# Kernel tuning notes

Measured on AMD Instinct MI355X. Metric: run time of the kernel, lower is better.

Reference implementation:

```python
import jax, jax.numpy as jnp
import numpy as np

B, E, F = 16384, 128, 6
ITEM_V, CATE_V, HIST = 91718, 11, 50
I_IDX, J_IDX = np.triu_indices(F, k=1)  # 15 field pairs, loop order (0,1),(0,2),...
EPS = 1e-5


def _xavier(key, shape):
    fan_in, fan_out = shape[0], shape[-1]
    std = (2.0 / (fan_in + fan_out)) ** 0.5
    return std * jax.random.normal(key, shape, dtype=jnp.float32)


def setup_inputs() -> dict:
    key = jax.random.key(0)
    ks = jax.random.split(key, 20)
    inp = {
        'item_id': jax.random.randint(ks[0], (B,), 0, ITEM_V),
        'item_emb_d128': jax.random.normal(ks[1], (B, 128), dtype=jnp.float32),
        'likes_level': jax.random.randint(ks[2], (B,), 0, CATE_V),
        'views_level': jax.random.randint(ks[3], (B,), 0, CATE_V),
        'item_seq': jax.random.randint(ks[4], (B, HIST), 0, ITEM_V),
        # learned parameters
        'item_emb': 0.05 * jax.random.normal(ks[5], (ITEM_V, E), dtype=jnp.float32),
        'cate_emb': 0.05 * jax.random.normal(ks[6], (CATE_V, E), dtype=jnp.float32),
        'mm_W': _xavier(ks[7], (128, E)), 'mm_b': jnp.zeros((E,), jnp.float32),
        'ln_g': jnp.ones((E,), jnp.float32), 'ln_b': jnp.zeros((E,), jnp.float32),
        'se_W1': _xavier(ks[8], (F, F // 2)), 'se_b1': jnp.zeros((F // 2,), jnp.float32),
        'se_W2': _xavier(ks[9], (F // 2, F)), 'se_b2': jnp.zeros((F,), jnp.float32),
        'bi_W': _xavier(ks[10], (E, E)),
        'mlp_W1': _xavier(ks[11], (21 * E, 512)), 'mlp_b1': jnp.zeros((512,), jnp.float32),
        'bn1_g': jnp.ones((512,), jnp.float32), 'bn1_b': jnp.zeros((512,), jnp.float32),
        'bn1_rm': jnp.zeros((512,), jnp.float32), 'bn1_rv': jnp.ones((512,), jnp.float32),
        'mlp_W2': _xavier(ks[12], (512, 256)), 'mlp_b2': jnp.zeros((256,), jnp.float32),
        'bn2_g': jnp.ones((256,), jnp.float32), 'bn2_b': jnp.zeros((256,), jnp.float32),
        'bn2_rm': jnp.zeros((256,), jnp.float32), 'bn2_rv': jnp.ones((256,), jnp.float32),
        'mlp_W3': _xavier(ks[13], (256, 1)), 'mlp_b3': jnp.zeros((1,), jnp.float32),
    }
    return inp


def _forward(item_id, item_emb_d128, likes_level, views_level, item_seq,
             item_emb, cate_emb, mm_W, mm_b, ln_g, ln_b,
             se_W1, se_b1, se_W2, se_b2, bi_W,
             mlp_W1, mlp_b1, bn1_g, bn1_b, bn1_rm, bn1_rv,
             mlp_W2, mlp_b2, bn2_g, bn2_b, bn2_rm, bn2_rv,
             mlp_W3, mlp_b3):
    b = item_id.shape[0]
    tab = item_emb.at[0].set(0.0)  # padding_idx=0
    like_feat = cate_emb[likes_level]
    view_feat = cate_emb[views_level]
    item_feat = tab[item_id]
    # mm_proj: Linear -> LayerNorm -> ReLU
    mm = item_emb_d128 @ mm_W + mm_b
    mu = mm.mean(-1, keepdims=True)
    var = jnp.var(mm, axis=-1, keepdims=True)
    mm = jax.nn.relu((mm - mu) / jnp.sqrt(var + EPS) * ln_g + ln_b)
    # masked mean pooling over history
    seq_emb = tab[item_seq]                               # (B, HIST, E)
    valid = (item_seq != 0).astype(seq_emb.dtype)
    seq_sum = (seq_emb * valid[..., None]).sum(1)
    cnt = jnp.clip(valid.sum(1, keepdims=True), 1.0)
    hist_feat = seq_sum / cnt
    user_feat = jnp.zeros((b, E), seq_emb.dtype)
    x = jnp.stack([user_feat, like_feat, view_feat, item_feat, mm, hist_feat], axis=1)  # (B,6,E)
    # SENet
    z = x.mean(-1)
    w = jax.nn.sigmoid(jax.nn.relu(z @ se_W1 + se_b1) @ se_W2 + se_b2)
    xs = x * w[:, :, None]
    # bilinear 'all'
    xw = jnp.einsum('bfe,ed->bfd', xs, bi_W)
    p = xs[:, I_IDX, :] * xw[:, J_IDX, :]                 # (B,15,E)
    c = jnp.concatenate([xs.reshape(b, -1), p.reshape(b, -1)], axis=1)  # (B, 2688)
    # MLP head (eval mode: BN uses running stats, dropout off)
    h = c @ mlp_W1 + mlp_b1
    h = jax.nn.relu((h - bn1_rm) / jnp.sqrt(bn1_rv + EPS) * bn1_g + bn1_b)
    h = h @ mlp_W2 + mlp_b2
    h = jax.nn.relu((h - bn2_rm) / jnp.sqrt(bn2_rv + EPS) * bn2_g + bn2_b)
    logits = h @ mlp_W3 + mlp_b3
    return jax.nn.sigmoid(logits)[:, 0]


def reference(item_id, item_emb_d128, likes_level, views_level, item_seq,
              item_emb, cate_emb, mm_W, mm_b, ln_g, ln_b,
              se_W1, se_b1, se_W2, se_b2, bi_W,
              mlp_W1, mlp_b1, bn1_g, bn1_b, bn1_rm, bn1_rv,
              mlp_W2, mlp_b2, bn2_g, bn2_b, bn2_rm, bn2_rv,
              mlp_W3, mlp_b3):
    return _forward(item_id, item_emb_d128, likes_level, views_level, item_seq,
                    item_emb, cate_emb, mm_W, mm_b, ln_g, ln_b,
                    se_W1, se_b1, se_W2, se_b2, bi_W,
                    mlp_W1, mlp_b1, bn1_g, bn1_b, bn1_rm, bn1_rv,
                    mlp_W2, mlp_b2, bn2_g, bn2_b, bn2_rm, bn2_rv,
                    mlp_W3, mlp_b3)
```

## Files before the change

kernel.cpp:

```cpp
#include <hip/hip_runtime.h>
#include <hip/hip_bf16.h>

typedef __hip_bfloat16 bfloat;
typedef __bf16 bf16x8 __attribute__((ext_vector_type(8)));
typedef float f32x4 __attribute__((ext_vector_type(4)));

#define B_SZ   16384
#define E_DIM  128
#define HIST_L 50


#define IPACK 0x3221110000ULL
#define JPACK 0x3323213210ULL

__device__ __forceinline__ void gl_lds16(const void* g, void* l) {
    __builtin_amdgcn_global_load_lds(
        (const __attribute__((address_space(1))) unsigned int*)g,
        (__attribute__((address_space(3))) unsigned int*)l, 16, 0, 0);
}

__device__ __forceinline__ bf16x8 mul_bf16x8(bf16x8 a, bf16x8 b) {
    union { bf16x8 v; __hip_bfloat162 h[4]; } ua, ub, ur;
    ua.v = a; ub.v = b;
    #pragma unroll
    for (int i = 0; i < 4; ++i) ur.h[i] = __hmul2(ua.h[i], ub.h[i]);
    return ur.v;
}

template<int TB>
__global__ __launch_bounds__(256) void feat_kernel(
    const int* __restrict__ item_id,
    const int* __restrict__ likes, const int* __restrict__ views,
    const int* __restrict__ seq,
    const void* __restrict__ item_tab, const float* __restrict__ cate_emb,
    const float* __restrict__ mm,
    const float* __restrict__ ln_g, const float* __restrict__ ln_b,
    const float* __restrict__ se_W1, const float* __restrict__ se_b1,
    const float* __restrict__ se_W2, const float* __restrict__ se_b2,
    bfloat* __restrict__ xs)
{
    const int tid = threadIdx.x;
    const int r   = tid >> 7;
    const int e   = tid & 127;
    const int b   = blockIdx.x * 2 + r;
    const int w   = tid >> 6;

    __shared__ float redh[2][4][128];
    __shared__ int   seq_s[2][64];
    __shared__ float lnred[4], lnred2[4];
    __shared__ float zred[5][4];
    __shared__ float wsh[2][6];
    __shared__ int   cnt_s[2];

    if (e < 64) seq_s[r][e] = (e < HIST_L) ? seq[(size_t)b * HIST_L + e] : 0;
    __syncthreads();

    const int iid = item_id[b];
    const float like_v = cate_emb[likes[b] * 128 + e];
    const float view_v = cate_emb[views[b] * 128 + e];
    float item_v;
    if (TB) {
        const bfloat* tb = (const bfloat*)item_tab;
        item_v = __bfloat162float(tb[(size_t)iid * 128 + e]);
    } else {
        const float* tf = (const float*)item_tab;
        float raw = tf[(size_t)iid * 128 + e];
        item_v = iid ? raw : 0.f;
    }
    const float acc = mm[(size_t)b * 128 + e];

    const int q   = e >> 5;
    const int l32 = e & 31;
    float4 hs = make_float4(0.f, 0.f, 0.f, 0.f);
    if (TB) {
        const ushort* tb = (const ushort*)item_tab;
        #pragma unroll
        for (int g = 0; g < 13; ++g) {
            int s = seq_s[r][g * 4 + q];
            ushort4 v = *(const ushort4*)&tb[(size_t)s * 128 + l32 * 4];
            hs.x += __bfloat162float(__ushort_as_bfloat16(v.x));
            hs.y += __bfloat162float(__ushort_as_bfloat16(v.y));
            hs.z += __bfloat162float(__ushort_as_bfloat16(v.z));
            hs.w += __bfloat162float(__ushort_as_bfloat16(v.w));
        }
    } else {
        const float* tf = (const float*)item_tab;
        #pragma unroll
        for (int g = 0; g < 13; ++g) {
            int s = seq_s[r][g * 4 + q];
            const float4 v = *(const float4*)&tf[(size_t)s * 128 + l32 * 4];
            float m = (s != 0) ? 1.f : 0.f;
            hs.x = fmaf(v.x, m, hs.x);
            hs.y = fmaf(v.y, m, hs.y);
            hs.z = fmaf(v.z, m, hs.z);
            hs.w = fmaf(v.w, m, hs.w);
        }
    }

    {
        float v = acc;
        #pragma unroll
        for (int off = 32; off > 0; off >>= 1) v += __shfl_down(v, off, 64);
        if ((tid & 63) == 0) lnred[w] = v;
    }
    __syncthreads();
    const float mu = (lnred[2 * r] + lnred[2 * r + 1]) * (1.f / 128.f);
    const float d  = acc - mu;
    {
        float v = d * d;
        #pragma unroll
        for (int off = 32; off > 0; off >>= 1) v += __shfl_down(v, off, 64);
        if ((tid & 63) == 0) lnred2[w] = v;
    }
    redh[r][q][l32 * 4 + 0] = hs.x;
    redh[r][q][l32 * 4 + 1] = hs.y;
    redh[r][q][l32 * 4 + 2] = hs.z;
    redh[r][q][l32 * 4 + 3] = hs.w;
    if ((w & 1) == 0 && e < 64) {
        bool valid = (e < HIST_L) && (seq_s[r][e] != 0);
        unsigned long long m = __ballot(valid);
        if (e == 0) cnt_s[r] = (int)__popcll(m);
    }
    __syncthreads();
    const float var = (lnred2[2 * r] + lnred2[2 * r + 1]) * (1.f / 128.f);
    float xmm = d * rsqrtf(var + 1e-5f) * ln_g[e] + ln_b[e];
    xmm = fmaxf(xmm, 0.f);

    const int cnt = cnt_s[r] > 0 ? cnt_s[r] : 1;
    const float hist_v = (redh[r][0][e] + redh[r][1][e] +
                          redh[r][2][e] + redh[r][3][e]) / (float)cnt;

    {
        float s1 = like_v, s2 = view_v, s3 = item_v, s4 = xmm, s5 = hist_v;
        #pragma unroll
        for (int off = 32; off > 0; off >>= 1) {
            s1 += __shfl_down(s1, off, 64);
            s2 += __shfl_down(s2, off, 64);
            s3 += __shfl_down(s3, off, 64);
            s4 += __shfl_down(s4, off, 64);
            s5 += __shfl_down(s5, off, 64);
        }
        if ((tid & 63) == 0) {
            zred[0][w] = s1; zred[1][w] = s2; zred[2][w] = s3;
            zred[3][w] = s4; zred[4][w] = s5;
        }
    }
    __syncthreads();

    if (e == 0) {
        float z[6];
        z[0] = 0.f;
        #pragma unroll
        for (int f = 1; f < 6; ++f)
            z[f] = (zred[f - 1][2 * r] + zred[f - 1][2 * r + 1]) * (1.f / 128.f);
        float a[3];
        #pragma unroll
        for (int j = 0; j < 3; ++j) {
            float s = se_b1[j];
            #pragma unroll
            for (int f = 0; f < 6; ++f) s += z[f] * se_W1[f * 3 + j];
            a[j] = fmaxf(s, 0.f);
        }
        #pragma unroll
        for (int f = 0; f < 6; ++f) {
            float s = se_b2[f];
            #pragma unroll
            for (int j = 0; j < 3; ++j) s += a[j] * se_W2[j * 6 + f];
            wsh[r][f] = 1.f / (1.f + expf(-s));
        }
    }
    __syncthreads();

    bfloat* xrow = xs + (size_t)b * 640;
    xrow[0 * 128 + e] = __float2bfloat16(like_v * wsh[r][1]);
    xrow[1 * 128 + e] = __float2bfloat16(view_v * wsh[r][2]);
    xrow[2 * 128 + e] = __float2bfloat16(item_v * wsh[r][3]);
    xrow[3 * 128 + e] = __float2bfloat16(xmm    * wsh[r][4]);
    xrow[4 * 128 + e] = __float2bfloat16(hist_v * wsh[r][5]);
}

__global__ __launch_bounds__(256) void transpose_f32_bf16(
    const float* __restrict__ in, bfloat* __restrict__ out, int K, int N)
{
    int idx = blockIdx.x * 256 + threadIdx.x;
    if (idx < K * N) {
        int k = idx / N, n = idx % N;
        out[(size_t)n * K + k] = __float2bfloat16(in[idx]);
    }
}

__global__ __launch_bounds__(256) void transpose_W1c(
    const float* __restrict__ W1, bfloat* __restrict__ W1t)
{
    int idx = blockIdx.x * 256 + threadIdx.x;
    if (idx < 512 * 1920) {
        int n = idx / 1920, kk = idx % 1920;
        int orig = kk + (kk < 640 ? 128 : 768);
        W1t[idx] = __float2bfloat16(W1[(size_t)orig * 512 + n]);
    }
}

__global__ __launch_bounds__(256) void cvt_f32_bf16(
    const float* __restrict__ in, bfloat* __restrict__ out, int n8)
{
    int idx = blockIdx.x * 256 + threadIdx.x;
    if (idx < n8) {
        float4 f0 = ((const float4*)in)[idx * 2];
        float4 f1 = ((const float4*)in)[idx * 2 + 1];
        union { bf16x8 v; unsigned short s[8]; } u;
        u.s[0] = __bfloat16_as_ushort(__float2bfloat16(f0.x));
        u.s[1] = __bfloat16_as_ushort(__float2bfloat16(f0.y));
        u.s[2] = __bfloat16_as_ushort(__float2bfloat16(f0.z));
        u.s[3] = __bfloat16_as_ushort(__float2bfloat16(f0.w));
        u.s[4] = __bfloat16_as_ushort(__float2bfloat16(f1.x));
        u.s[5] = __bfloat16_as_ushort(__float2bfloat16(f1.y));
        u.s[6] = __bfloat16_as_ushort(__float2bfloat16(f1.z));
        u.s[7] = __bfloat16_as_ushort(__float2bfloat16(f1.w));
        ((bf16x8*)out)[idx] = u.v;
    }
}

__global__ __launch_bounds__(256) void cvt_emb(
    const float* __restrict__ in, bfloat* __restrict__ out, int n8)
{
    int idx = blockIdx.x * 256 + threadIdx.x;
    if (idx >= n8) return;
    if (idx < 16) {
        union { bf16x8 v; unsigned short s[8]; } z;
        #pragma unroll
        for (int i = 0; i < 8; ++i) z.s[i] = 0;
        ((bf16x8*)out)[idx] = z.v;
        return;
    }
    float4 f0 = ((const float4*)in)[idx * 2];
    float4 f1 = ((const float4*)in)[idx * 2 + 1];
    union { bf16x8 v; unsigned short s[8]; } u;
    u.s[0] = __bfloat16_as_ushort(__float2bfloat16(f0.x));
    u.s[1] = __bfloat16_as_ushort(__float2bfloat16(f0.y));
    u.s[2] = __bfloat16_as_ushort(__float2bfloat16(f0.z));
    u.s[3] = __bfloat16_as_ushort(__float2bfloat16(f0.w));
    u.s[4] = __bfloat16_as_ushort(__float2bfloat16(f1.x));
    u.s[5] = __bfloat16_as_ushort(__float2bfloat16(f1.y));
    u.s[6] = __bfloat16_as_ushort(__float2bfloat16(f1.z));
    u.s[7] = __bfloat16_as_ushort(__float2bfloat16(f1.w));
    ((bf16x8*)out)[idx] = u.v;
}

__global__ __launch_bounds__(256) void pair_kernel(
    const bfloat* __restrict__ xs, const bfloat* __restrict__ xw,
    bfloat* __restrict__ P, int total)
{
    int idx = blockIdx.x * 256 + threadIdx.x;
    if (idx >= total) return;
    int b = idx / 160, c = idx % 160;
    int pp = c >> 4, q = c & 15;
    int isl = (int)((IPACK >> (4 * pp)) & 15);
    int jsl = (int)((JPACK >> (4 * pp)) & 15);
    bf16x8 a = *(const bf16x8*)&xs[(size_t)b * 640 + isl * 128 + q * 8];
    bf16x8 w = *(const bf16x8*)&xw[((size_t)b * 4 + jsl) * 128 + q * 8];
    *(bf16x8*)&P[(size_t)b * 1280 + c * 8] = mul_bf16x8(a, w);
}

__global__ __launch_bounds__(256) void bn_pre(
    const float* __restrict__ lb1, const float* __restrict__ g1,
    const float* __restrict__ bb1, const float* __restrict__ rm1,
    const float* __restrict__ rv1,
    const float* __restrict__ lb2, const float* __restrict__ g2,
    const float* __restrict__ bb2, const float* __restrict__ rm2,
    const float* __restrict__ rv2,
    const float* __restrict__ mm_b,
    float* __restrict__ S1, float* __restrict__ T1,
    float* __restrict__ S2, float* __restrict__ T2,
    float* __restrict__ Tmm)
{
    int j = blockIdx.x * 256 + threadIdx.x;
    if (j < 512) {
        float s = g1[j] * rsqrtf(rv1[j] + 1e-5f);
        S1[j] = s;
        T1[j] = (lb1[j] - rm1[j]) * s + bb1[j];
    } else if (j < 768) {
        int k = j - 512;
        float s = g2[k] * rsqrtf(rv2[k] + 1e-5f);
        S2[k] = s;
        T2[k] = (lb2[k] - rm2[k]) * s + bb2[k];
    } else if (j < 896) {
        Tmm[j - 768] = mm_b[j - 768];
    }
}

template<int MODE, int EPI, int F32OUT>
__global__ __launch_bounds__(256) void gemm_bt(
    const void* __restrict__ A, const bfloat* __restrict__ A2,
    const bfloat* __restrict__ Bt, void* __restrict__ C,
    int M, int N, int K,
    const float* __restrict__ S, const float* __restrict__ T)
{
    __shared__ __align__(16) short As[3][64 * 64];
    __shared__ __align__(16) short Bs[3][64 * 64];

    const int tid  = threadIdx.x;
    const int bm   = blockIdx.x * 64;
    const int bn   = blockIdx.y * 64;
    const int wave = tid >> 6;
    const int lane = tid & 63;
    const int wm   = (wave >> 1) * 32;
    const int wn   = (wave & 1) * 32;

    const short* Ag  = (const short*)A;
    const short* A2g = (const short*)A2;
    const short* Bg  = (const short*)Bt;

    f32x4 acc[2][2];
    #pragma unroll
    for (int i = 0; i < 2; ++i)
        #pragma unroll
        for (int j = 0; j < 2; ++j)
            acc[i][j] = (f32x4){0.f, 0.f, 0.f, 0.f};

    const int srow = tid >> 3;
    const int sck  = tid & 7;

    auto stage = [&](int buf, int kt) {
        #pragma unroll
        for (int rr = 0; rr < 2; ++rr) {
            int row = srow + rr * 32;
            int g   = sck ^ (row & 7);
            gl_lds16(&Bg[(long)(bn + row) * K + kt + g * 8],
                     &Bs[buf][row * 64 + sck * 8]);
        }
        #pragma unroll
        for (int rr = 0; rr < 2; ++rr) {
            int row = srow + rr * 32;
            int g   = sck ^ (row & 7);
            const short* src;
            if (MODE == 4) {
                long rb = (long)(bm + row);
                src = (kt < 640)
                    ? &Ag [rb * 640  + kt + g * 8]
                    : &A2g[rb * 1280 + (kt - 640) + g * 8];
            } else if (MODE == 2) {
                int gr = bm + row;
                src = &Ag[((long)(gr >> 2)) * 640 +
                          ((gr & 3) + 1) * 128 + kt + g * 8];
            } else {
                src = &Ag[(long)(bm + row) * K + kt + g * 8];
            }
            gl_lds16(src, &As[buf][row * 64 + sck * 8]);
        }
    };

    const int rbase = lane & 15;
    const int cswz  = rbase & 7;

    const int nk = K >> 6;
    stage(0, 0);
    stage(1, 64);

    for (int i = 0; i < nk; ++i) {
        if (i + 1 < nk) asm volatile("s_waitcnt vmcnt(4)" ::: "memory");
        else            asm volatile("s_waitcnt vmcnt(0)" ::: "memory");
        __builtin_amdgcn_s_barrier();
        __builtin_amdgcn_sched_barrier(0);

        const int cur = i % 3;
        #pragma unroll
        for (int h = 0; h < 2; ++h) {
            const int cg = h * 4 + (lane >> 4);
            const int ca = (cg ^ cswz) << 3;
            bf16x8 af[2], bfr[2];
            #pragma unroll
            for (int mt = 0; mt < 2; ++mt)
                af[mt] = *(const bf16x8*)
                    &As[cur][(wm + mt * 16 + rbase) * 64 + ca];
            #pragma unroll
            for (int nt = 0; nt < 2; ++nt)
                bfr[nt] = *(const bf16x8*)
                    &Bs[cur][(wn + nt * 16 + rbase) * 64 + ca];
            #pragma unroll
            for (int mt = 0; mt < 2; ++mt)
                #pragma unroll
                for (int nt = 0; nt < 2; ++nt)
                    acc[mt][nt] = __builtin_amdgcn_mfma_f32_16x16x32_bf16(
                        af[mt], bfr[nt], acc[mt][nt], 0, 0, 0);
        }

        if (i + 2 < nk) stage((i + 2) % 3, (i + 2) << 6);
    }

    const int col0 = lane & 15;
    const int row0 = (lane >> 4) * 4;
    #pragma unroll
    for (int nt = 0; nt < 2; ++nt) {
        int col = bn + wn + nt * 16 + col0;
        float s = 1.f, t = 0.f;
        if (EPI) { s = (EPI == 1) ? S[col] : 1.f; t = T[col]; }
        #pragma unroll
        for (int mt = 0; mt < 2; ++mt) {
            #pragma unroll
            for (int i = 0; i < 4; ++i) {
                int row = bm + wm + mt * 16 + row0 + i;
                float v = acc[mt][nt][i];
                if (EPI == 1) v = fmaxf(v * s + t, 0.f);
                if (EPI == 2) v = v + t;
                if (F32OUT) ((float*)C)[(size_t)row * N + col] = v;
                else ((bfloat*)C)[(size_t)row * N + col] = __float2bfloat16(v);
            }
        }
    }
}

__global__ __launch_bounds__(256) void head_kernel(
    const bfloat* __restrict__ h2, const float* __restrict__ W3,
    const float* __restrict__ b3, float* __restrict__ out)
{
    int lane = threadIdx.x & 63;
    int row  = blockIdx.x * 4 + (threadIdx.x >> 6);
    float acc = 0.f;
    #pragma unroll
    for (int i = 0; i < 4; ++i)
        acc += __bfloat162float(h2[(size_t)row * 256 + i * 64 + lane]) *
               W3[i * 64 + lane];
    #pragma unroll
    for (int off = 32; off > 0; off >>= 1) acc += __shfl_down(acc, off, 64);
    if (lane == 0) {
        float l = acc + b3[0];
        out[row] = 1.f / (1.f + expf(-l));
    }
}

extern "C" void kernel_launch(void* const* d_in, const int* in_sizes, int n_in,
                              void* d_out, int out_size, void* d_ws, size_t ws_size,
                              hipStream_t stream) {
    const int*   item_id = (const int*)  d_in[0];
    const float* d128    = (const float*)d_in[1];
    const int*   likes   = (const int*)  d_in[2];
    const int*   views   = (const int*)  d_in[3];
    const int*   seq     = (const int*)  d_in[4];
    const float* item_emb= (const float*)d_in[5];
    const float* cate_emb= (const float*)d_in[6];
    const float* mm_W    = (const float*)d_in[7];
    const float* mm_b    = (const float*)d_in[8];
    const float* ln_g    = (const float*)d_in[9];
    const float* ln_b    = (const float*)d_in[10];
    const float* se_W1   = (const float*)d_in[11];
    const float* se_b1   = (const float*)d_in[12];
    const float* se_W2   = (const float*)d_in[13];
    const float* se_b2   = (const float*)d_in[14];
    const float* bi_W    = (const float*)d_in[15];
    const float* W1      = (const float*)d_in[16];
    const float* b1      = (const float*)d_in[17];
    const float* bn1_g   = (const float*)d_in[18];
    const float* bn1_b   = (const float*)d_in[19];
    const float* bn1_rm  = (const float*)d_in[20];
    const float* bn1_rv  = (const float*)d_in[21];
    const float* W2      = (const float*)d_in[22];
    const float* b2      = (const float*)d_in[23];
    const float* bn2_g   = (const float*)d_in[24];
    const float* bn2_b   = (const float*)d_in[25];
    const float* bn2_rm  = (const float*)d_in[26];
    const float* bn2_rv  = (const float*)d_in[27];
    const float* W3      = (const float*)d_in[28];
    const float* b3      = (const float*)d_in[29];

    const size_t fixed = 2300416;
    const size_t ITB   = 23479808;
    int CH; bool use_tb;
    if      (fixed + ITB + (size_t)8192 * 4864 <= ws_size) { CH = 8192; use_tb = true;  }
    else if (fixed + ITB + (size_t)4096 * 4864 <= ws_size) { CH = 4096; use_tb = true;  }
    else if (fixed + (size_t)8192 * 4864 <= ws_size)       { CH = 8192; use_tb = false; }
    else if (fixed + (size_t)4096 * 4864 <= ws_size)       { CH = 4096; use_tb = false; }
    else if (fixed + (size_t)2048 * 4864 <= ws_size)       { CH = 2048; use_tb = false; }
    else                                                   { CH = 1024; use_tb = false; }

    char* ws = (char*)d_ws;
    bfloat* W1t = (bfloat*)(ws);
    bfloat* W2t = (bfloat*)(ws + 1966080);
    bfloat* bWt = (bfloat*)(ws + 2228224);
    bfloat* mmWt= (bfloat*)(ws + 2260992);
    float*  S1  = (float*) (ws + 2293760);
    float*  T1  = (float*) (ws + 2295808);
    float*  S2  = (float*) (ws + 2297856);
    float*  T2  = (float*) (ws + 2298880);
    float*  Tmm = (float*) (ws + 2299904);
    bfloat* itemb = (bfloat*)(ws + fixed);
    char*   cb  = ws + fixed + (use_tb ? ITB : 0);
    bfloat* xs  = (bfloat*)(cb);
    bfloat* xw  = (bfloat*)(cb + (size_t)CH * 1280);
    bfloat* h1  = xw;
    bfloat* P   = (bfloat*)(cb + (size_t)CH * 2304);
    bfloat* d128b = (bfloat*)P;
    float*  mm  = (float*)((char*)P + (size_t)CH * 256);
    bfloat* h2  = (bfloat*)P;

    transpose_W1c<<<(512 * 1920 + 255) / 256, 256, 0, stream>>>(W1, W1t);
    transpose_f32_bf16<<<(512 * 256 + 255) / 256, 256, 0, stream>>>(W2, W2t, 512, 256);
    transpose_f32_bf16<<<(128 * 128 + 255) / 256, 256, 0, stream>>>(bi_W, bWt, 128, 128);
    transpose_f32_bf16<<<(128 * 128 + 255) / 256, 256, 0, stream>>>(mm_W, mmWt, 128, 128);
    bn_pre<<<4, 256, 0, stream>>>(b1, bn1_g, bn1_b, bn1_rm, bn1_rv,
                                  b2, bn2_g, bn2_b, bn2_rm, bn2_rv,
                                  mm_b, S1, T1, S2, T2, Tmm);
    if (use_tb) {
        const int n8 = 91718 * 128 / 8;
        cvt_emb<<<(n8 + 255) / 256, 256, 0, stream>>>(item_emb, itemb, n8);
    }

    for (int off = 0; off < B_SZ; off += CH) {
        cvt_f32_bf16<<<(CH * 16 + 255) / 256, 256, 0, stream>>>(
            d128 + (size_t)off * 128, d128b, CH * 16);

        dim3 gmm(CH / 64, 2);
        gemm_bt<0, 2, 1><<<gmm, 256, 0, stream>>>(
            d128b, nullptr, mmWt, mm, CH, 128, 128, nullptr, Tmm);

        if (use_tb)
            feat_kernel<1><<<CH / 2, 256, 0, stream>>>(
                item_id + off, likes + off, views + off,
                seq + (size_t)off * HIST_L, itemb, cate_emb, mm,
                ln_g, ln_b, se_W1, se_b1, se_W2, se_b2, xs);
        else
            feat_kernel<0><<<CH / 2, 256, 0, stream>>>(
                item_id + off, likes + off, views + off,
                seq + (size_t)off * HIST_L, item_emb, cate_emb, mm,
                ln_g, ln_b, se_W1, se_b1, se_W2, se_b2, xs);

        dim3 gxw(CH * 4 / 64, 2);
        gemm_bt<2, 0, 0><<<gxw, 256, 0, stream>>>(
            xs, nullptr, bWt, xw, CH * 4, 128, 128, nullptr, nullptr);

        pair_kernel<<<(CH * 160 + 255) / 256, 256, 0, stream>>>(
            xs, xw, P, CH * 160);

        dim3 g1(CH / 64, 8);
        gemm_bt<4, 1, 0><<<g1, 256, 0, stream>>>(
            xs, P, W1t, h1, CH, 512, 1920, S1, T1);

        dim3 g2(CH / 64, 4);
        gemm_bt<0, 1, 0><<<g2, 256, 0, stream>>>(
            h1, nullptr, W2t, h2, CH, 256, 512, S2, T2);

        head_kernel<<<CH / 4, 256, 0, stream>>>(h2, W3, b3, (float*)d_out + off);
    }
}
```

Before: 333.9 us.

## Fuse weight prep kernels, fold fp32 conversion into GEMM, enlarge batch chunk

Merges the three weight transposes and the BN precompute into one prep kernel, cutting launch count. Removes the separate fp32-to-bf16 conversion pass by adding a GEMM mode that loads fp32 A directly, converts it in registers and writes it to LDS. The chunk-size selection now tries the whole batch (16384) first, so the per-chunk loop can run once when the workspace allows. The new GEMM mode drops async global-to-LDS loads for A and waits fully each iteration, which weakens pipelining in that small GEMM.

```diff
diff --git a/kernel.cpp b/kernel.cpp
--- a/kernel.cpp
+++ b/kernel.cpp
@@ -179,16 +179,6 @@
     xrow[4 * 128 + e] = __float2bfloat16(hist_v * wsh[r][5]);
 }
 
-__global__ __launch_bounds__(256) void transpose_f32_bf16(
-    const float* __restrict__ in, bfloat* __restrict__ out, int K, int N)
-{
-    int idx = blockIdx.x * 256 + threadIdx.x;
-    if (idx < K * N) {
-        int k = idx / N, n = idx % N;
-        out[(size_t)n * K + k] = __float2bfloat16(in[idx]);
-    }
-}
-
 __global__ __launch_bounds__(256) void transpose_W1c(
     const float* __restrict__ W1, bfloat* __restrict__ W1t)
 {
@@ -200,23 +190,47 @@
     }
 }
 
-__global__ __launch_bounds__(256) void cvt_f32_bf16(
-    const float* __restrict__ in, bfloat* __restrict__ out, int n8)
+__global__ __launch_bounds__(256) void prep_kernel(
+    const float* __restrict__ W2, const float* __restrict__ bi_W,
+    const float* __restrict__ mm_W,
+    bfloat* __restrict__ W2t, bfloat* __restrict__ bWt,
+    bfloat* __restrict__ mmWt,
+    const float* __restrict__ lb1, const float* __restrict__ g1,
+    const float* __restrict__ bb1, const float* __restrict__ rm1,
+    const float* __restrict__ rv1,
+    const float* __restrict__ lb2, const float* __restrict__ g2,
+    const float* __restrict__ bb2, const float* __restrict__ rm2,
+    const float* __restrict__ rv2,
+    const float* __restrict__ mm_b,
+    float* __restrict__ S1, float* __restrict__ T1,
+    float* __restrict__ S2, float* __restrict__ T2,
+    float* __restrict__ Tmm)
 {
     int idx = blockIdx.x * 256 + threadIdx.x;
-    if (idx < n8) {
-        float4 f0 = ((const float4*)in)[idx * 2];
-        float4 f1 = ((const float4*)in)[idx * 2 + 1];
-        union { bf16x8 v; unsigned short s[8]; } u;
-        u.s[0] = __bfloat16_as_ushort(__float2bfloat16(f0.x));
-        u.s[1] = __bfloat16_as_ushort(__float2bfloat16(f0.y));
-        u.s[2] = __bfloat16_as_ushort(__float2bfloat16(f0.z));
-        u.s[3] = __bfloat16_as_ushort(__float2bfloat16(f0.w));
-        u.s[4] = __bfloat16_as_ushort(__float2bfloat16(f1.x));
-        u.s[5] = __bfloat16_as_ushort(__float2bfloat16(f1.y));
-        u.s[6] = __bfloat16_as_ushort(__float2bfloat16(f1.z));
-        u.s[7] = __bfloat16_as_ushort(__float2bfloat16(f1.w));
-        ((bf16x8*)out)[idx] = u.v;
+    if (idx < 131072) {
+        int k = idx >> 8, n = idx & 255;
+        W2t[(size_t)n * 512 + k] = __float2bfloat16(W2[idx]);
+    } else if (idx < 147456) {
+        int t = idx - 131072;
+        int k = t >> 7, n = t & 127;
+        bWt[n * 128 + k] = __float2bfloat16(bi_W[t]);
+    } else if (idx < 163840) {
+        int t = idx - 147456;
+        int k = t >> 7, n = t & 127;
+        mmWt[n * 128 + k] = __float2bfloat16(mm_W[t]);
+    } else if (idx < 164352) {
+        int j = idx - 163840;
+        float s = g1[j] * rsqrtf(rv1[j] + 1e-5f);
+        S1[j] = s;
+        T1[j] = (lb1[j] - rm1[j]) * s + bb1[j];
+    } else if (idx < 164608) {
+        int j = idx - 164352;
+        float s = g2[j] * rsqrtf(rv2[j] + 1e-5f);
+        S2[j] = s;
+        T2[j] = (lb2[j] - rm2[j]) * s + bb2[j];
+    } else if (idx < 164736) {
+        int j = idx - 164608;
+        Tmm[j] = mm_b[j];
     }
 }
 
@@ -261,33 +275,6 @@
     *(bf16x8*)&P[(size_t)b * 1280 + c * 8] = mul_bf16x8(a, w);
 }
 
-__global__ __launch_bounds__(256) void bn_pre(
-    const float* __restrict__ lb1, const float* __restrict__ g1,
-    const float* __restrict__ bb1, const float* __restrict__ rm1,
-    const float* __restrict__ rv1,
-    const float* __restrict__ lb2, const float* __restrict__ g2,
-    const float* __restrict__ bb2, const float* __restrict__ rm2,
-    const float* __restrict__ rv2,
-    const float* __restrict__ mm_b,
-    float* __restrict__ S1, float* __restrict__ T1,
-    float* __restrict__ S2, float* __restrict__ T2,
-    float* __restrict__ Tmm)
-{
-    int j = blockIdx.x * 256 + threadIdx.x;
-    if (j < 512) {
-        float s = g1[j] * rsqrtf(rv1[j] + 1e-5f);
-        S1[j] = s;
-        T1[j] = (lb1[j] - rm1[j]) * s + bb1[j];
-    } else if (j < 768) {
-        int k = j - 512;
-        float s = g2[k] * rsqrtf(rv2[k] + 1e-5f);
-        S2[k] = s;
-        T2[k] = (lb2[k] - rm2[k]) * s + bb2[k];
-    } else if (j < 896) {
-        Tmm[j - 768] = mm_b[j - 768];
-    }
-}
-
 template<int MODE, int EPI, int F32OUT>
 __global__ __launch_bounds__(256) void gemm_bt(
     const void* __restrict__ A, const bfloat* __restrict__ A2,
@@ -328,24 +315,46 @@
             gl_lds16(&Bg[(long)(bn + row) * K + kt + g * 8],
                      &Bs[buf][row * 64 + sck * 8]);
         }
-        #pragma unroll
-        for (int rr = 0; rr < 2; ++rr) {
-            int row = srow + rr * 32;
-            int g   = sck ^ (row & 7);
-            const short* src;
-            if (MODE == 4) {
-                long rb = (long)(bm + row);
-                src = (kt < 640)
-                    ? &Ag [rb * 640  + kt + g * 8]
-                    : &A2g[rb * 1280 + (kt - 640) + g * 8];
-            } else if (MODE == 2) {
-                int gr = bm + row;
-                src = &Ag[((long)(gr >> 2)) * 640 +
-                          ((gr & 3) + 1) * 128 + kt + g * 8];
-            } else {
-                src = &Ag[(long)(bm + row) * K + kt + g * 8];
+        if (MODE == 3) {
+            const float* Af = (const float*)A;
+            #pragma unroll
+            for (int rr = 0; rr < 2; ++rr) {
+                int row = srow + rr * 32;
+                int g   = sck ^ (row & 7);
+                long aoff = (long)(bm + row) * K + kt + g * 8;
+                float4 f0 = *(const float4*)&Af[aoff];
+                float4 f1 = *(const float4*)&Af[aoff + 4];
+                union { bf16x8 v; unsigned short s[8]; } u;
+                u.s[0] = __bfloat16_as_ushort(__float2bfloat16(f0.x));
+                u.s[1] = __bfloat16_as_ushort(__float2bfloat16(f0.y));
+                u.s[2] = __bfloat16_as_ushort(__float2bfloat16(f0.z));
+                u.s[3] = __bfloat16_as_ushort(__float2bfloat16(f0.w));
+                u.s[4] = __bfloat16_as_ushort(__float2bfloat16(f1.x));
+                u.s[5] = __bfloat16_as_ushort(__float2bfloat16(f1.y));
+                u.s[6] = __bfloat16_as_ushort(__float2bfloat16(f1.z));
+                u.s[7] = __bfloat16_as_ushort(__float2bfloat16(f1.w));
+                *(bf16x8*)&As[buf][row * 64 + sck * 8] = u.v;
             }
-            gl_lds16(src, &As[buf][row * 64 + sck * 8]);
+        } else {
+            #pragma unroll
+            for (int rr = 0; rr < 2; ++rr) {
+                int row = srow + rr * 32;
+                int g   = sck ^ (row & 7);
+                const short* src;
+                if (MODE == 4) {
+                    long rb = (long)(bm + row);
+                    src = (kt < 640)
+                        ? &Ag [rb * 640  + kt + g * 8]
+                        : &A2g[rb * 1280 + (kt - 640) + g * 8];
+                } else if (MODE == 2) {
+                    int gr = bm + row;
+                    src = &Ag[((long)(gr >> 2)) * 640 +
+                              ((gr & 3) + 1) * 128 + kt + g * 8];
+                } else {
+                    src = &Ag[(long)(bm + row) * K + kt + g * 8];
+                }
+                gl_lds16(src, &As[buf][row * 64 + sck * 8]);
+            }
         }
     };
 
@@ -357,8 +366,12 @@
     stage(1, 64);
 
     for (int i = 0; i < nk; ++i) {
-        if (i + 1 < nk) asm volatile("s_waitcnt vmcnt(4)" ::: "memory");
-        else            asm volatile("s_waitcnt vmcnt(0)" ::: "memory");
+        if (MODE == 3)
+            asm volatile("s_waitcnt vmcnt(0) lgkmcnt(0)" ::: "memory");
+        else if (i + 1 < nk)
+            asm volatile("s_waitcnt vmcnt(4)" ::: "memory");
+        else
+            asm volatile("s_waitcnt vmcnt(0)" ::: "memory");
         __builtin_amdgcn_s_barrier();
         __builtin_amdgcn_sched_barrier(0);
 
@@ -465,12 +478,14 @@
     const size_t fixed = 2300416;
     const size_t ITB   = 23479808;
     int CH; bool use_tb;
-    if      (fixed + ITB + (size_t)8192 * 4864 <= ws_size) { CH = 8192; use_tb = true;  }
-    else if (fixed + ITB + (size_t)4096 * 4864 <= ws_size) { CH = 4096; use_tb = true;  }
-    else if (fixed + (size_t)8192 * 4864 <= ws_size)       { CH = 8192; use_tb = false; }
-    else if (fixed + (size_t)4096 * 4864 <= ws_size)       { CH = 4096; use_tb = false; }
-    else if (fixed + (size_t)2048 * 4864 <= ws_size)       { CH = 2048; use_tb = false; }
-    else                                                   { CH = 1024; use_tb = false; }
+    if      (fixed + ITB + (size_t)16384 * 4864 <= ws_size) { CH = 16384; use_tb = true;  }
+    else if (fixed + (size_t)16384 * 4864 <= ws_size)       { CH = 16384; use_tb = false; }
+    else if (fixed + ITB + (size_t)8192 * 4864 <= ws_size)  { CH = 8192;  use_tb = true;  }
+    else if (fixed + (size_t)8192 * 4864 <= ws_size)        { CH = 8192;  use_tb = false; }
+    else if (fixed + ITB + (size_t)4096 * 4864 <= ws_size)  { CH = 4096;  use_tb = true;  }
+    else if (fixed + (size_t)4096 * 4864 <= ws_size)        { CH = 4096;  use_tb = false; }
+    else if (fixed + (size_t)2048 * 4864 <= ws_size)        { CH = 2048;  use_tb = false; }
+    else                                                    { CH = 1024;  use_tb = false; }
 
     char* ws = (char*)d_ws;
     bfloat* W1t = (bfloat*)(ws);
@@ -488,29 +503,25 @@
     bfloat* xw  = (bfloat*)(cb + (size_t)CH * 1280);
     bfloat* h1  = xw;
     bfloat* P   = (bfloat*)(cb + (size_t)CH * 2304);
-    bfloat* d128b = (bfloat*)P;
-    float*  mm  = (float*)((char*)P + (size_t)CH * 256);
+    float*  mm  = (float*)P;
     bfloat* h2  = (bfloat*)P;
 
     transpose_W1c<<<(512 * 1920 + 255) / 256, 256, 0, stream>>>(W1, W1t);
-    transpose_f32_bf16<<<(512 * 256 + 255) / 256, 256, 0, stream>>>(W2, W2t, 512, 256);
-    transpose_f32_bf16<<<(128 * 128 + 255) / 256, 256, 0, stream>>>(bi_W, bWt, 128, 128);
-    transpose_f32_bf16<<<(128 * 128 + 255) / 256, 256, 0, stream>>>(mm_W, mmWt, 128, 128);
-    bn_pre<<<4, 256, 0, stream>>>(b1, bn1_g, bn1_b, bn1_rm, bn1_rv,
-                                  b2, bn2_g, bn2_b, bn2_rm, bn2_rv,
-                                  mm_b, S1, T1, S2, T2, Tmm);
+    prep_kernel<<<(164736 + 255) / 256, 256, 0, stream>>>(
+        W2, bi_W, mm_W, W2t, bWt, mmWt,
+        b1, bn1_g, bn1_b, bn1_rm, bn1_rv,
+        b2, bn2_g, bn2_b, bn2_rm, bn2_rv,
+        mm_b, S1, T1, S2, T2, Tmm);
     if (use_tb) {
         const int n8 = 91718 * 128 / 8;
         cvt_emb<<<(n8 + 255) / 256, 256, 0, stream>>>(item_emb, itemb, n8);
     }
 
     for (int off = 0; off < B_SZ; off += CH) {
-        cvt_f32_bf16<<<(CH * 16 + 255) / 256, 256, 0, stream>>>(
-            d128 + (size_t)off * 128, d128b, CH * 16);
-
         dim3 gmm(CH / 64, 2);
-        gemm_bt<0, 2, 1><<<gmm, 256, 0, stream>>>(
-            d128b, nullptr, mmWt, mm, CH, 128, 128, nullptr, Tmm);
+        gemm_bt<3, 2, 1><<<gmm, 256, 0, stream>>>(
+            d128 + (size_t)off * 128, nullptr, mmWt, mm,
+            CH, 128, 128, nullptr, Tmm);
 
         if (use_tb)
             feat_kernel<1><<<CH / 2, 256, 0, stream>>>(
```

Result: faster. 291.4 us (-12.7%).
